# Optimization experiments

Measured on AMD Instinct MI355X. Metric: run time of the kernel, lower is better.

## Reference

```python
import jax, jax.numpy as jnp
import numpy as np

I = 128   # input_size
H = 256   # state_size


def setup_inputs() -> dict:
    key = jax.random.key(0)
    ks = jax.random.split(key, 7)
    T, B = 512, 1024
    # Xavier-ish init scales for params
    s_ih = 1.0 / np.sqrt(I)
    s_hh = 1.0 / np.sqrt(H)
    return {
        "x":    jax.random.normal(ks[0], (T, B, I), dtype=jnp.float32),
        "W_ih": jax.random.normal(ks[1], (4 * H, I), dtype=jnp.float32) * s_ih,
        "W_hh": jax.random.normal(ks[2], (4 * H, H), dtype=jnp.float32) * s_hh,
        "b_ih": jax.random.normal(ks[3], (4 * H,), dtype=jnp.float32) * s_hh,
        "b_hh": jax.random.normal(ks[4], (4 * H,), dtype=jnp.float32) * s_hh,
        "hx0":  jax.random.normal(ks[5], (H,), dtype=jnp.float32) * s_hh,
        "cx0":  jax.random.normal(ks[6], (H,), dtype=jnp.float32) * s_hh,
    }


def _lstm_forward(x, W_ih, W_hh, b_ih, b_hh, hx0, cx0):
    T, B, _ = x.shape
    past_length = T - 1  # use_last_past=False
    x_used = x[:past_length]
    # Precompute input projections for all steps at once: [T-1, B, 4H]
    x_proj = jnp.einsum("tbi,gi->tbg", x_used, W_ih) + b_ih + b_hh

    h0 = jnp.broadcast_to(hx0, (B, H))
    c0 = jnp.broadcast_to(cx0, (B, H))

    def step(carry, xp):
        h, c = carry
        gates = xp + h @ W_hh.T  # [B, 4H]
        i_g, f_g, g_g, o_g = jnp.split(gates, 4, axis=-1)
        i_g = jax.nn.sigmoid(i_g)
        f_g = jax.nn.sigmoid(f_g)
        g_g = jnp.tanh(g_g)
        o_g = jax.nn.sigmoid(o_g)
        c_new = f_g * c + i_g * g_g
        h_new = o_g * jnp.tanh(c_new)
        return (h_new, c_new), None

    (h, c), _ = jax.lax.scan(step, (h0, c0), x_proj)
    return h, c


def reference(x, W_ih, W_hh, b_ih, b_hh, hx0, cx0):
    return _lstm_forward(x, W_ih, W_hh, b_ih, b_hh, hx0, cx0)
```

## Files before the change

### kernel.cpp

```cpp
#include <hip/hip_runtime.h>
#include <hip/hip_bf16.h>


#define T_STEPS 511
#define BATCH   1024
#define IN      128
#define HID     256
#define NG      1024
#define KTOT    384
#define BWG     16
#define NGROUP  64
#define SW      264
#define HS      264

typedef __bf16 bf16x8 __attribute__((ext_vector_type(8)));
typedef float  f32x4  __attribute__((ext_vector_type(4)));
typedef unsigned long long u64;

#define WCAT_OFF 0
#define BIAS_OFF 786432
#define HEXG_OFF 790528
#define CNT_OFF  1839104

__global__ void precast_kernel(const float* __restrict__ W_ih,
                               const float* __restrict__ W_hh,
                               const float* __restrict__ b_ih,
                               const float* __restrict__ b_hh,
                               __bf16* __restrict__ wcat,
                               float* __restrict__ bias,
                               int* __restrict__ cnt) {
    int idx = blockIdx.x * blockDim.x + threadIdx.x;
    if (idx < NG * KTOT) {
        int n = idx / KTOT, k = idx % KTOT;
        float v = (k < IN) ? W_ih[n * IN + k] : W_hh[n * HID + (k - IN)];
        wcat[idx] = (__bf16)v;
    }
    if (idx < NG) bias[idx] = b_ih[idx] + b_hh[idx];
    if (idx < NGROUP * 32) cnt[idx] = 0;
}

__device__ __forceinline__ float sigmoidf_fast(float v) {
    return 1.f / (1.f + __expf(-v));
}
__device__ __forceinline__ float tanhf_fast(float v) {
    return 1.f - 2.f / (1.f + __expf(2.f * v));
}

#define MFMA(a, b, c) __builtin_amdgcn_mfma_f32_16x16x32_bf16((a), (b), (c), 0, 0, 0)

__device__ __forceinline__ bf16x8 cvt_pack(float4 lo, float4 hi) {
    return bf16x8{(__bf16)lo.x, (__bf16)lo.y, (__bf16)lo.z, (__bf16)lo.w,
                  (__bf16)hi.x, (__bf16)hi.y, (__bf16)hi.z, (__bf16)hi.w};
}

__global__ __launch_bounds__(512, 2) void lstm_kernel(
    const float* __restrict__ x,
    const __bf16* __restrict__ wcat,
    const float* __restrict__ bias,
    const float* __restrict__ hx0,
    const float* __restrict__ cx0,
    __bf16* __restrict__ hexg,
    int* __restrict__ cnt,
    float* __restrict__ out)
{
    __shared__ alignas(16) __bf16 Whh[256 * SW];
    __shared__ alignas(16) __bf16 Ah[BWG * HS];

    const int tid  = threadIdx.x;
    const int bx   = blockIdx.x;
    const int g    = bx & 63;
    const int s    = bx >> 6;
    const int wave = tid >> 6;
    const int lane = tid & 63;
    const int col  = lane & 15;
    const int quad = lane >> 4;
    const int hf   = col >> 3;
    const int b0   = g * BWG;
    const int j0   = s * 64;
    const int jcol = j0 + wave * 8 + (col & 7);

    int* cntg = cnt + g * 32;

    {
        int r  = tid >> 1;
        int hh = (tid & 1) * 128;
        int ngl = ((r >> 6) << 8) + j0 + (r & 63);
        const __bf16* src = wcat + (size_t)ngl * KTOT + IN + hh;
        __bf16* dst = &Whh[r * SW + hh];
        #pragma unroll
        for (int i = 0; i < 16; ++i)
            *(bf16x8*)(dst + i * 8) = *(const bf16x8*)(src + i * 8);
    }

    const int n0 = (hf ? 256 : 0) + jcol;
    const int n1 = 512 + (hf ? 256 : 0) + jcol;
    bf16x8 wi0[4], wi1[4];
    #pragma unroll
    for (int ks = 0; ks < 4; ++ks) {
        wi0[ks] = *(const bf16x8*)(wcat + (size_t)n0 * KTOT + ks * 32 + quad * 8);
        wi1[ks] = *(const bf16x8*)(wcat + (size_t)n1 * KTOT + ks * 32 + quad * 8);
    }

    const float bi  = bias[jcol];
    const float bfv = bias[256 + jcol];
    const float bg  = bias[512 + jcol];
    const float bo  = bias[768 + jcol];

    float cst[4], hn[4];
    {
        float cv = cx0[jcol];
        #pragma unroll
        for (int r = 0; r < 4; ++r) cst[r] = cv;
    }

    float4 x0f[8], xf[8];
    #pragma unroll
    for (int ks = 0; ks < 4; ++ks) {
        const float* xp = x + (size_t)(b0 + col) * IN + ks * 32 + quad * 8;
        x0f[2 * ks]     = *(const float4*)xp;
        x0f[2 * ks + 1] = *(const float4*)(xp + 4);
        const float* xq = xp + (size_t)BATCH * IN;
        xf[2 * ks]      = *(const float4*)xq;
        xf[2 * ks + 1]  = *(const float4*)(xq + 4);
    }

    const int nl0 = hf * 64 + wave * 8 + (col & 7);
    const __bf16* wl0 = &Whh[nl0 * SW + quad * 8];
    const __bf16* wl1 = &Whh[(128 + nl0) * SW + quad * 8];

    __syncthreads();

    f32x4 aA0 = {0.f,0.f,0.f,0.f}, aA1 = {0.f,0.f,0.f,0.f};
    f32x4 aB0 = {0.f,0.f,0.f,0.f}, aB1 = {0.f,0.f,0.f,0.f};
    {
        bf16x8 ax[4];
        #pragma unroll
        for (int ks = 0; ks < 4; ++ks)
            ax[ks] = cvt_pack(x0f[2 * ks], x0f[2 * ks + 1]);
        aA0 = MFMA(ax[0], wi0[0], aA0); aB0 = MFMA(ax[0], wi1[0], aB0);
        aA1 = MFMA(ax[1], wi0[1], aA1); aB1 = MFMA(ax[1], wi1[1], aB1);
        aA0 = MFMA(ax[2], wi0[2], aA0); aB0 = MFMA(ax[2], wi1[2], aB0);
        aA1 = MFMA(ax[3], wi0[3], aA1); aB1 = MFMA(ax[3], wi1[3], aB1);
    }

    for (int t = 0; t < T_STEPS; ++t) {
        bf16x8 ahf[8];
        if (t == 0) {
            #pragma unroll
            for (int ks = 0; ks < 8; ++ks) {
                const float* hp = hx0 + ks * 32 + quad * 8;
                ahf[ks] = cvt_pack(*(const float4*)hp, *(const float4*)(hp + 4));
            }
        } else {
            const int target = 32 * t;
            int guard = 0;
            while (__hip_atomic_load(cntg, __ATOMIC_RELAXED,
                                     __HIP_MEMORY_SCOPE_AGENT) < target) {
                __builtin_amdgcn_s_sleep(1);
                if (++guard > (1 << 22)) break;
            }
            const u64* sp = (const u64*)(hexg
                + ((size_t)((t & 1) * NGROUP + g)) * (BWG * HID)) + tid * 2;
            u64 v0 = __hip_atomic_load(sp,     __ATOMIC_RELAXED, __HIP_MEMORY_SCOPE_AGENT);
            u64 v1 = __hip_atomic_load(sp + 1, __ATOMIC_RELAXED, __HIP_MEMORY_SCOPE_AGENT);
            int row = tid >> 5, c8 = (tid & 31) * 8;
            *(u64*)&Ah[row * HS + c8]     = v0;
            *(u64*)&Ah[row * HS + c8 + 4] = v1;
            __syncthreads();
            #pragma unroll
            for (int ks = 0; ks < 8; ++ks)
                ahf[ks] = *(const bf16x8*)&Ah[col * HS + ks * 32 + quad * 8];
        }

        #pragma unroll
        for (int ks = 0; ks < 4; ++ks) {
            bf16x8 w0a = *(const bf16x8*)(wl0 + ks * 32);
            bf16x8 w1a = *(const bf16x8*)(wl1 + ks * 32);
            bf16x8 w0b = *(const bf16x8*)(wl0 + (ks + 4) * 32);
            bf16x8 w1b = *(const bf16x8*)(wl1 + (ks + 4) * 32);
            aA0 = MFMA(ahf[ks],     w0a, aA0);
            aB0 = MFMA(ahf[ks],     w1a, aB0);
            aA1 = MFMA(ahf[ks + 4], w0b, aA1);
            aB1 = MFMA(ahf[ks + 4], w1b, aB1);
        }
        f32x4 accA = aA0 + aA1;
        f32x4 accB = aB0 + aB1;

        #pragma unroll
        for (int r = 0; r < 4; ++r) {
            float oA = __shfl_xor(accA[r], 8, 64);
            float oB = __shfl_xor(accB[r], 8, 64);
            float iv = (hf ? oA : accA[r]) + bi;
            float fv = (hf ? accA[r] : oA) + bfv;
            float gv = (hf ? oB : accB[r]) + bg;
            float ov = (hf ? accB[r] : oB) + bo;
            float ig = sigmoidf_fast(iv);
            float fg = sigmoidf_fast(fv);
            float gt = tanhf_fast(gv);
            float og = sigmoidf_fast(ov);
            float cn = fg * cst[r] + ig * gt;
            cst[r] = cn;
            hn[r]  = og * tanhf_fast(cn);
        }

        if (t < T_STEPS - 1) {
            __bf16* base = hexg
                + ((size_t)((((t + 1) & 1) * NGROUP) + g)) * (BWG * HID);
            #pragma unroll
            for (int r = 0; r < 4; ++r) {
                unsigned short mine;
                {
                    __bf16 hv = (__bf16)hn[r];
                    __builtin_memcpy(&mine, &hv, 2);
                }
                int other = __shfl_xor((int)mine, 1, 64);
                if ((col & 1) == 0 && col < 8) {
                    unsigned int val = (unsigned int)mine
                                     | ((unsigned int)(unsigned short)other << 16);
                    unsigned int* p = (unsigned int*)(base
                        + (size_t)(quad * 4 + r) * HID + jcol);
                    __hip_atomic_store(p, val, __ATOMIC_RELAXED,
                                       __HIP_MEMORY_SCOPE_AGENT);
                }
            }
            asm volatile("s_waitcnt vmcnt(0)" ::: "memory");
            if (lane == 0)
                __hip_atomic_fetch_add(cntg, 1, __ATOMIC_RELAXED,
                                       __HIP_MEMORY_SCOPE_AGENT);

            {
                bf16x8 ax[4];
                #pragma unroll
                for (int ks = 0; ks < 4; ++ks)
                    ax[ks] = cvt_pack(xf[2 * ks], xf[2 * ks + 1]);
                aA0 = {0.f,0.f,0.f,0.f}; aA1 = {0.f,0.f,0.f,0.f};
                aB0 = {0.f,0.f,0.f,0.f}; aB1 = {0.f,0.f,0.f,0.f};
                aA0 = MFMA(ax[0], wi0[0], aA0); aB0 = MFMA(ax[0], wi1[0], aB0);
                aA1 = MFMA(ax[1], wi0[1], aA1); aB1 = MFMA(ax[1], wi1[1], aB1);
                aA0 = MFMA(ax[2], wi0[2], aA0); aB0 = MFMA(ax[2], wi1[2], aB0);
                aA1 = MFMA(ax[3], wi0[3], aA1); aB1 = MFMA(ax[3], wi1[3], aB1);
            }
            if (t + 2 <= T_STEPS - 1) {
                #pragma unroll
                for (int ks = 0; ks < 4; ++ks) {
                    const float* xp = x + (size_t)(t + 2) * BATCH * IN
                                    + (size_t)(b0 + col) * IN + ks * 32 + quad * 8;
                    xf[2 * ks]     = *(const float4*)xp;
                    xf[2 * ks + 1] = *(const float4*)(xp + 4);
                }
            }
        }
    }

    if (col < 8) {
        #pragma unroll
        for (int r = 0; r < 4; ++r) {
            int row = b0 + quad * 4 + r;
            out[(size_t)row * HID + jcol] = hn[r];
            out[(size_t)BATCH * HID + (size_t)row * HID + jcol] = cst[r];
        }
    }
}

extern "C" void kernel_launch(void* const* d_in, const int* in_sizes, int n_in,
                              void* d_out, int out_size, void* d_ws, size_t ws_size,
                              hipStream_t stream) {
    const float* x    = (const float*)d_in[0];
    const float* W_ih = (const float*)d_in[1];
    const float* W_hh = (const float*)d_in[2];
    const float* b_ih = (const float*)d_in[3];
    const float* b_hh = (const float*)d_in[4];
    const float* hx0  = (const float*)d_in[5];
    const float* cx0  = (const float*)d_in[6];
    float* outp = (float*)d_out;

    __bf16* wcat = (__bf16*)((char*)d_ws + WCAT_OFF);
    float*  bias = (float*)((char*)d_ws + BIAS_OFF);
    __bf16* hexg = (__bf16*)((char*)d_ws + HEXG_OFF);
    int*    cnt  = (int*)((char*)d_ws + CNT_OFF);

    precast_kernel<<<dim3((NG * KTOT + 255) / 256), dim3(256), 0, stream>>>(
        W_ih, W_hh, b_ih, b_hh, wcat, bias, cnt);

    void* args[] = {(void*)&x, (void*)&wcat, (void*)&bias, (void*)&hx0,
                    (void*)&cx0, (void*)&hexg, (void*)&cnt, (void*)&outp};
    hipLaunchCooperativeKernel((const void*)lstm_kernel, dim3(256), dim3(512),
                               args, 0, stream);
}
```

Measured before the change: 2.979 ms.

## Replace counter barrier with epoch-tagged hidden-state exchange polling

Each exchanged bf16 hidden value is now stored as a 32-bit word whose upper 16 bits carry the timestep epoch. Consumers poll the data words directly until every epoch tag matches, instead of waiting on a per-group atomic counter. This removes the producer's vmcnt wait and atomic fetch_add from the per-step critical path. In exchange it doubles the bytes exchanged, adds tag-unpacking work and an extra __syncthreads, and relies on stale workspace contents never carrying a matching tag.

Result: slower. 3.572 ms (+19.9%).

```diff
diff --git a/kernel.cpp b/kernel.cpp
--- a/kernel.cpp
+++ b/kernel.cpp
@@ -16,19 +16,19 @@
 typedef __bf16 bf16x8 __attribute__((ext_vector_type(8)));
 typedef float  f32x4  __attribute__((ext_vector_type(4)));
 typedef unsigned long long u64;
+typedef unsigned int u32;
+typedef u32 u32x4 __attribute__((ext_vector_type(4)));
 
 #define WCAT_OFF 0
 #define BIAS_OFF 786432
 #define HEXG_OFF 790528
-#define CNT_OFF  1839104
 
 __global__ void precast_kernel(const float* __restrict__ W_ih,
                                const float* __restrict__ W_hh,
                                const float* __restrict__ b_ih,
                                const float* __restrict__ b_hh,
                                __bf16* __restrict__ wcat,
-                               float* __restrict__ bias,
-                               int* __restrict__ cnt) {
+                               float* __restrict__ bias) {
     int idx = blockIdx.x * blockDim.x + threadIdx.x;
     if (idx < NG * KTOT) {
         int n = idx / KTOT, k = idx % KTOT;
@@ -36,7 +36,6 @@
         wcat[idx] = (__bf16)v;
     }
     if (idx < NG) bias[idx] = b_ih[idx] + b_hh[idx];
-    if (idx < NGROUP * 32) cnt[idx] = 0;
 }
 
 __device__ __forceinline__ float sigmoidf_fast(float v) {
@@ -59,8 +58,7 @@
     const float* __restrict__ bias,
     const float* __restrict__ hx0,
     const float* __restrict__ cx0,
-    __bf16* __restrict__ hexg,
-    int* __restrict__ cnt,
+    u32* __restrict__ hexg,
     float* __restrict__ out)
 {
     __shared__ alignas(16) __bf16 Whh[256 * SW];
@@ -79,8 +77,6 @@
     const int j0   = s * 64;
     const int jcol = j0 + wave * 8 + (col & 7);
 
-    int* cntg = cnt + g * 32;
-
     {
         int r  = tid >> 1;
         int hh = (tid & 1) * 128;
@@ -152,24 +148,34 @@
                 ahf[ks] = cvt_pack(*(const float4*)hp, *(const float4*)(hp + 4));
             }
         } else {
-            const int target = 32 * t;
+            const u64* sp = (const u64*)hexg
+                + ((size_t)((t & 1) * NGROUP + g)) * (BWG * HID / 2) + tid * 4;
+            const u64 et = ((u64)(u32)t << 16) | ((u64)(u32)t << 48);
+            u64 v0, v1, v2, v3;
             int guard = 0;
-            while (__hip_atomic_load(cntg, __ATOMIC_RELAXED,
-                                     __HIP_MEMORY_SCOPE_AGENT) < target) {
+            for (;;) {
+                v0 = __hip_atomic_load(sp + 0, __ATOMIC_RELAXED, __HIP_MEMORY_SCOPE_AGENT);
+                v1 = __hip_atomic_load(sp + 1, __ATOMIC_RELAXED, __HIP_MEMORY_SCOPE_AGENT);
+                v2 = __hip_atomic_load(sp + 2, __ATOMIC_RELAXED, __HIP_MEMORY_SCOPE_AGENT);
+                v3 = __hip_atomic_load(sp + 3, __ATOMIC_RELAXED, __HIP_MEMORY_SCOPE_AGENT);
+                u64 bad = ((v0 ^ et) | (v1 ^ et) | (v2 ^ et) | (v3 ^ et))
+                        & 0xFFFF0000FFFF0000ull;
+                if (bad == 0) break;
+                if (++guard > (1 << 18)) break;
                 __builtin_amdgcn_s_sleep(1);
-                if (++guard > (1 << 22)) break;
-            }
-            const u64* sp = (const u64*)(hexg
-                + ((size_t)((t & 1) * NGROUP + g)) * (BWG * HID)) + tid * 2;
-            u64 v0 = __hip_atomic_load(sp,     __ATOMIC_RELAXED, __HIP_MEMORY_SCOPE_AGENT);
-            u64 v1 = __hip_atomic_load(sp + 1, __ATOMIC_RELAXED, __HIP_MEMORY_SCOPE_AGENT);
+            }
             int row = tid >> 5, c8 = (tid & 31) * 8;
-            *(u64*)&Ah[row * HS + c8]     = v0;
-            *(u64*)&Ah[row * HS + c8 + 4] = v1;
+            u32x4 pk;
+            pk.x = (u32)(v0 & 0xFFFF) | ((u32)((v0 >> 32) & 0xFFFF) << 16);
+            pk.y = (u32)(v1 & 0xFFFF) | ((u32)((v1 >> 32) & 0xFFFF) << 16);
+            pk.z = (u32)(v2 & 0xFFFF) | ((u32)((v2 >> 32) & 0xFFFF) << 16);
+            pk.w = (u32)(v3 & 0xFFFF) | ((u32)((v3 >> 32) & 0xFFFF) << 16);
+            *(u32x4*)&Ah[row * HS + c8] = pk;
             __syncthreads();
             #pragma unroll
             for (int ks = 0; ks < 8; ++ks)
                 ahf[ks] = *(const bf16x8*)&Ah[col * HS + ks * 32 + quad * 8];
+            __syncthreads();
         }
 
         #pragma unroll
@@ -204,29 +210,19 @@
         }
 
         if (t < T_STEPS - 1) {
-            __bf16* base = hexg
-                + ((size_t)((((t + 1) & 1) * NGROUP) + g)) * (BWG * HID);
-            #pragma unroll
-            for (int r = 0; r < 4; ++r) {
-                unsigned short mine;
-                {
+            if (col < 8) {
+                u32* base = hexg
+                    + ((size_t)(((t + 1) & 1) * NGROUP + g)) * (BWG * HID) + jcol;
+                const u32 ep = ((u32)(t + 1)) << 16;
+                #pragma unroll
+                for (int r = 0; r < 4; ++r) {
                     __bf16 hv = (__bf16)hn[r];
-                    __builtin_memcpy(&mine, &hv, 2);
+                    unsigned short hb;
+                    __builtin_memcpy(&hb, &hv, 2);
+                    __hip_atomic_store(base + (quad * 4 + r) * HID, (u32)hb | ep,
+                                       __ATOMIC_RELAXED, __HIP_MEMORY_SCOPE_AGENT);
                 }
-                int other = __shfl_xor((int)mine, 1, 64);
-                if ((col & 1) == 0 && col < 8) {
-                    unsigned int val = (unsigned int)mine
-                                     | ((unsigned int)(unsigned short)other << 16);
-                    unsigned int* p = (unsigned int*)(base
-                        + (size_t)(quad * 4 + r) * HID + jcol);
-                    __hip_atomic_store(p, val, __ATOMIC_RELAXED,
-                                       __HIP_MEMORY_SCOPE_AGENT);
-                }
-            }
-            asm volatile("s_waitcnt vmcnt(0)" ::: "memory");
-            if (lane == 0)
-                __hip_atomic_fetch_add(cntg, 1, __ATOMIC_RELAXED,
-                                       __HIP_MEMORY_SCOPE_AGENT);
+            }
 
             {
                 bf16x8 ax[4];
@@ -276,14 +272,13 @@
 
     __bf16* wcat = (__bf16*)((char*)d_ws + WCAT_OFF);
     float*  bias = (float*)((char*)d_ws + BIAS_OFF);
-    __bf16* hexg = (__bf16*)((char*)d_ws + HEXG_OFF);
-    int*    cnt  = (int*)((char*)d_ws + CNT_OFF);
+    u32*    hexg = (u32*)((char*)d_ws + HEXG_OFF);
 
     precast_kernel<<<dim3((NG * KTOT + 255) / 256), dim3(256), 0, stream>>>(
-        W_ih, W_hh, b_ih, b_hh, wcat, bias, cnt);
+        W_ih, W_hh, b_ih, b_hh, wcat, bias);
 
     void* args[] = {(void*)&x, (void*)&wcat, (void*)&bias, (void*)&hx0,
-                    (void*)&cx0, (void*)&hexg, (void*)&cnt, (void*)&outp};
+                    (void*)&cx0, (void*)&hexg, (void*)&outp};
     hipLaunchCooperativeKernel((const void*)lstm_kernel, dim3(256), dim3(512),
                                args, 0, stream);
 }
```
